# Optimization experiments

Hardware: AMD Instinct MI355X
Metric: run time of the kernel (lower is better)

Reference implementation:

```python
import jax, jax.numpy as jnp
import numpy as np

MAX_DIST = 20
N_HEADS = 8
LN_EPS = 1e-5


def _layer_norm(x, g, b):
    mu = jnp.mean(x, axis=-1, keepdims=True)
    var = jnp.var(x, axis=-1, keepdims=True)
    return (x - mu) / jnp.sqrt(var + LN_EPS) * g + b


def setup_inputs() -> dict:
    key = jax.random.key(0)
    ks = jax.random.split(key, 12)
    B, N, D, H, F = 8, 1024, 768, N_HEADS, 1024
    w = lambda k, *sh: (jax.random.normal(k, sh, jnp.float32) * 0.02)
    return {
        "x": jax.random.normal(ks[0], (B, N, D), jnp.float32),
        "node_mask": jnp.ones((B, N), jnp.int32),
        "centers": jnp.arange(B * N, dtype=jnp.float32).reshape(B, N),
        "types": jax.random.randint(ks[1], (B, N), 0, 2, jnp.int32),
        # params (torch Linear weights stored transposed as [in, out])
        "qkv_w": w(ks[2], D, 3 * D), "qkv_b": jnp.zeros((3 * D,), jnp.float32),
        "out_w": w(ks[3], D, D), "out_b": jnp.zeros((D,), jnp.float32),
        "ff1_w": w(ks[4], D, F), "ff1_b": jnp.zeros((F,), jnp.float32),
        "ff2_w": w(ks[5], F, D), "ff2_b": jnp.zeros((D,), jnp.float32),
        "ln1_g": jnp.ones((D,), jnp.float32), "ln1_b": jnp.zeros((D,), jnp.float32),
        "ln2_g": jnp.ones((D,), jnp.float32), "ln2_b": jnp.zeros((D,), jnp.float32),
        "rel_emb": w(ks[6], 2 * MAX_DIST + 1, H),  # relative-distance bias table
        "tt": w(ks[7], H, 2, 2),                   # type-pair bias table
    }


def reference(x, node_mask, centers, types,
              qkv_w, qkv_b, out_w, out_b,
              ff1_w, ff1_b, ff2_w, ff2_b,
              ln1_g, ln1_b, ln2_g, ln2_b,
              rel_emb, tt):
    B, N, D = x.shape
    H = rel_emb.shape[1]
    Dh = D // H

    qkv = x @ qkv_w + qkv_b                       # [B,N,3D]
    q, k, v = jnp.split(qkv, 3, axis=-1)
    split = lambda t: t.reshape(B, N, H, Dh).transpose(0, 2, 1, 3)  # [B,H,N,Dh]
    q, k, v = split(q), split(k), split(v)

    scores = jnp.einsum("bhid,bhjd->bhij", q, k) / np.sqrt(Dh).astype(np.float32)

    # relative-position bias: bucket clamped distance into [0, 2*max_dist]
    dist = centers[:, :, None] - centers[:, None, :]              # [B,N,N]
    idx = jnp.round(jnp.clip(dist, -MAX_DIST, MAX_DIST) + MAX_DIST).astype(jnp.int32)
    rb = rel_emb[idx].transpose(0, 3, 1, 2)                       # [B,H,N,N]

    # type-pair bias
    ti = jnp.broadcast_to(types[:, :, None], (B, N, N))
    tj = jnp.broadcast_to(types[:, None, :], (B, N, N))
    tb = tt[:, ti, tj].transpose(1, 0, 2, 3)                      # [B,H,N,N]

    scores = scores + rb + tb
    mask = node_mask[:, None, None, :]                            # [B,1,1,N]
    scores = jnp.where(mask == 0, -jnp.inf, scores)
    att = jax.nn.softmax(scores, axis=-1)
    att = jnp.nan_to_num(att, nan=0.0)

    y = jnp.einsum("bhij,bhjd->bhid", att, v)
    y = y.transpose(0, 2, 1, 3).reshape(B, N, D)
    y = y @ out_w + out_b

    x = _layer_norm(x + y, ln1_g, ln1_b)
    ff = jax.nn.gelu(x @ ff1_w + ff1_b, approximate=False) @ ff2_w + ff2_b
    x = _layer_norm(x + ff, ln2_g, ln2_b)
    return x
```

## Files before the change

### kernel.cpp

```cpp
#include <hip/hip_runtime.h>

typedef short short8 __attribute__((ext_vector_type(8)));
typedef unsigned short ushort8v __attribute__((ext_vector_type(8)));
typedef float f32x4 __attribute__((ext_vector_type(4)));

static __device__ __forceinline__ unsigned short f2b(float f) {
    unsigned int u = __builtin_bit_cast(unsigned int, f);
    unsigned int r = (u + 0x7fffu + ((u >> 16) & 1u)) >> 16;
    return (unsigned short)r;
}
static __device__ __forceinline__ unsigned short f2b_trunc(float f) {
    return (unsigned short)(__builtin_bit_cast(unsigned int, f) >> 16);
}
static __device__ __forceinline__ float b2f(unsigned short u) {
    return __builtin_bit_cast(float, (unsigned int)u << 16);
}
static __device__ __forceinline__ float exp2v(float x) {
    float r;
    asm("v_exp_f32 %0, %1" : "=v"(r) : "v"(x));
    return r;
}

__device__ __forceinline__ void gload16(void* lds, const void* g) {
    __builtin_amdgcn_global_load_lds(
        (const __attribute__((address_space(1))) void*)g,
        (__attribute__((address_space(3))) void*)lds, 16, 0, 0);
}

#define L2E 1.4426950408889634f

__global__ __launch_bounds__(256) void cvt_x_kernel(const float* __restrict__ x,
                                                    unsigned short* __restrict__ o, int n4) {
    int i = blockIdx.x * 256 + threadIdx.x;
    float4 f = ((const float4*)x)[i];
    ushort4 u;
    u.x = f2b(f.x); u.y = f2b(f.y); u.z = f2b(f.z); u.w = f2b(f.w);
    ((ushort4*)o)[i] = u;
}

__global__ __launch_bounds__(256) void transpose_w(const float* __restrict__ W,
                                                   unsigned short* __restrict__ Wt,
                                                   int K, int N) {
    __shared__ float t[32][33];
    int kb = blockIdx.y << 5, nb = blockIdx.x << 5;
    int tx = threadIdx.x & 31, ty = threadIdx.x >> 5;
#pragma unroll
    for (int i = 0; i < 32; i += 8)
        t[ty + i][tx] = W[(size_t)(kb + ty + i) * N + nb + tx];
    __syncthreads();
#pragma unroll
    for (int i = 0; i < 32; i += 8)
        Wt[(size_t)(nb + ty + i) * K + kb + tx] = f2b(t[tx][ty + i]);
}

__global__ __launch_bounds__(256) void aug_qk(const int* __restrict__ types,
                                              const int* __restrict__ nmask,
                                              const float* __restrict__ tt,
                                              unsigned short* __restrict__ Qb,
                                              unsigned short* __restrict__ Kb) {
    int t = blockIdx.x * 256 + threadIdx.x;
    int bh = t >> 10, n = t & 1023;
    int b = bh >> 3, h = bh & 7;
    int tj = types[b * 1024 + n];
    int mk = nmask[b * 1024 + n];
    float t00 = tt[h * 4], t01 = tt[h * 4 + 1], t10 = tt[h * 4 + 2], t11 = tt[h * 4 + 3];
    float bA = L2E * (t00 + (t01 - t00) * tj) + (mk ? 0.f : -1e30f);
    float bB = L2E * ((t10 - t00) + (t11 - t01 - t10 + t00) * tj);
    size_t off = ((size_t)bh * 1024 + n) * 128 + 96;
    ushort8v z = {0, 0, 0, 0, 0, 0, 0, 0};
    ushort8v qv = z, kv = z;
    qv[0] = 0x3F80u;
    qv[1] = tj ? 0x3F80u : 0u;
    kv[0] = f2b(bA);
    kv[1] = f2b(bB);
    *(ushort8v*)&Qb[off] = qv;
    *(ushort8v*)&Qb[off + 8] = z;
    *(ushort8v*)&Qb[off + 16] = z;
    *(ushort8v*)&Qb[off + 24] = z;
    *(ushort8v*)&Kb[off] = kv;
    *(ushort8v*)&Kb[off + 8] = z;
    *(ushort8v*)&Kb[off + 16] = z;
    *(ushort8v*)&Kb[off + 24] = z;
}

template <int EPI>
__global__ __launch_bounds__(512, 4) void gemm2p(
    const unsigned short* __restrict__ A, const unsigned short* __restrict__ Bt,
    const float* __restrict__ bias, float* __restrict__ outf,
    unsigned short* __restrict__ outb, unsigned short* __restrict__ q_o,
    unsigned short* __restrict__ k_o, unsigned short* __restrict__ v_o,
    int N, int K, int ntn, int NT) {
    __shared__ unsigned short a_lds[2][8192];
    __shared__ unsigned short b_lds[2][8192];
    const int tid = threadIdx.x;
    const int wave = tid >> 6, lane = tid & 63;
    const int lr = lane & 15, lg = lane >> 4;
    const int wm = wave >> 2, wn = wave & 3;
    const int nwg = gridDim.x;
    const int orig = blockIdx.x;
    const int swz = (orig & 7) * (nwg >> 3) + (orig >> 3);
    const int tm = swz / ntn, tn = swz % ntn;

    const unsigned short* srcA[2];
    const unsigned short* srcB[2];
#pragma unroll
    for (int i = 0; i < 2; ++i) {
        int g = i * 512 + tid;
        int row = g >> 3, sl = g & 7;
        int colg = sl ^ (row & 7);
        srcA[i] = A + (size_t)(tm * 128 + row) * K + colg * 8;
        srcB[i] = Bt + (size_t)(tn * 128 + row) * K + colg * 8;
    }
    auto stage = [&](int buf, int k0) {
#pragma unroll
        for (int i = 0; i < 2; ++i) {
            gload16(&a_lds[buf][i * 4096 + wave * 512], srcA[i] + k0);
            gload16(&b_lds[buf][i * 4096 + wave * 512], srcB[i] + k0);
        }
    };

    f32x4 acc[4][2] = {};

    stage(0, 0);
    asm volatile("s_waitcnt vmcnt(0)" ::: "memory");
    __builtin_amdgcn_s_barrier();

    for (int t = 0; t < NT; ++t) {
        const int buf = t & 1;
        if (t + 1 < NT) stage(buf ^ 1, (t + 1) * 64);
#pragma unroll
        for (int ks = 0; ks < 2; ++ks) {
            short8 af[4], bfr[2];
#pragma unroll
            for (int mf = 0; mf < 4; ++mf) {
                int row = wm * 64 + mf * 16 + lr;
                int slot = (ks * 4 + lg) ^ (row & 7);
                af[mf] = *(const short8*)&a_lds[buf][row * 64 + slot * 8];
            }
#pragma unroll
            for (int nf = 0; nf < 2; ++nf) {
                int row = wn * 32 + nf * 16 + lr;
                int slot = (ks * 4 + lg) ^ (row & 7);
                bfr[nf] = *(const short8*)&b_lds[buf][row * 64 + slot * 8];
            }
#pragma unroll
            for (int mf = 0; mf < 4; ++mf)
#pragma unroll
                for (int nf = 0; nf < 2; ++nf)
                    acc[mf][nf] = __builtin_amdgcn_mfma_f32_16x16x32_bf16(af[mf], bfr[nf], acc[mf][nf], 0, 0, 0);
        }
        asm volatile("s_waitcnt vmcnt(0)" ::: "memory");
        __builtin_amdgcn_s_barrier();
    }

#pragma unroll
    for (int nf = 0; nf < 2; ++nf) {
        int gc = tn * 128 + wn * 32 + nf * 16 + lr;
        float bv = bias[gc];
        int part = 0, h = 0, dh = 0;
        if constexpr (EPI == 3) {
            part = gc / 768;
            int cc = gc - part * 768;
            h = cc / 96;
            dh = cc - h * 96;
        }
#pragma unroll
        for (int mf = 0; mf < 4; ++mf) {
            int grb = tm * 128 + wm * 64 + mf * 16 + lg * 4;
            if constexpr (EPI == 3) {
                int b = grb >> 10, n2 = grb & 1023;
                size_t bh = (size_t)(b * 8 + h);
                if (part == 2) {
                    ushort4 wv;
                    wv.x = f2b(acc[mf][nf][0] + bv);
                    wv.y = f2b(acc[mf][nf][1] + bv);
                    wv.z = f2b(acc[mf][nf][2] + bv);
                    wv.w = f2b(acc[mf][nf][3] + bv);
                    *(ushort4*)&v_o[(bh * 96 + dh) * 1024 + n2] = wv;
                } else {
                    unsigned short* dst = (part == 0) ? q_o : k_o;
                    float sc = (part == 0) ? 0.14724445f : 1.f;
#pragma unroll
                    for (int r = 0; r < 4; ++r)
                        dst[(bh * 1024 + n2 + r) * 128 + dh] = f2b((acc[mf][nf][r] + bv) * sc);
                }
            } else {
#pragma unroll
                for (int r = 0; r < 4; ++r) {
                    int gr = grb + r;
                    float v = acc[mf][nf][r] + bv;
                    if constexpr (EPI == 0) {
                        outf[(size_t)gr * N + gc] = v;
                    } else if constexpr (EPI == 1) {
                        outb[(size_t)gr * N + gc] = f2b(v);
                    } else {
                        float gl = 0.5f * v * (1.f + erff(v * 0.70710678f));
                        outb[(size_t)gr * N + gc] = f2b(gl);
                    }
                }
            }
        }
    }
}

__global__ __launch_bounds__(512, 4) void attn_kernel(
    const unsigned short* __restrict__ Qb, const unsigned short* __restrict__ Kb,
    const unsigned short* __restrict__ Vt, const float* __restrict__ centers,
    const float* __restrict__ rel_emb, unsigned short* __restrict__ Y) {
    __shared__ unsigned short kv_lds[2 * 14336];
    __shared__ unsigned short p_lds[8 * 1024];
    __shared__ float c_lds[1024];
    __shared__ float rel_lds[41];

    const int tid = threadIdx.x;
    const int wave = tid >> 6, lane = tid & 63;
    const int lr = lane & 15, lg = lane >> 4;
    const int bh = blockIdx.x, qb = blockIdx.y;
    const int b = bh >> 3, h = bh & 7;
    const int q0 = qb * 128 + wave * 16;
    const size_t kvbase = (size_t)bh * 1024 * 128;

    c_lds[tid] = centers[b * 1024 + tid];
    c_lds[tid + 512] = centers[b * 1024 + 512 + tid];
    if (tid < 41) rel_lds[tid] = rel_emb[tid * 8 + h] * L2E;

    const unsigned short* sbase[4];
    int sstep[4];
#pragma unroll
    for (int it = 0; it < 4; ++it) {
        int g = (it < 3) ? it * 512 + tid : 1536 + wave * 64 + lane;
        if (g < 1024) {
            int ks = g >> 8, rem = g & 255, pr = rem >> 3, sl = rem & 7;
            int so = sl ^ (pr & 7);
            int r = ((so >> 2) << 5) + pr, oct = so & 3;
            sbase[it] = Kb + kvbase + (size_t)r * 128 + ks * 32 + oct * 8;
            sstep[it] = 64 * 128;
        } else {
            int v = g - 1024, pr = v >> 3, sl = v & 7;
            int so = sl ^ (pr & 7);
            sbase[it] = Vt + (size_t)(bh * 96 + (pr < 96 ? pr : 95)) * 1024 + so * 8;
            sstep[it] = 64;
        }
    }
    auto stage = [&](int bufb, int kt) {
        unsigned short* dst = kv_lds + bufb * 14336;
#pragma unroll
        for (int it = 0; it < 3; ++it)
            gload16(dst + it * 4096 + wave * 512, sbase[it] + (size_t)kt * sstep[it]);
        if (tid < 256)
            gload16(dst + 3 * 4096 + wave * 512, sbase[3] + (size_t)kt * sstep[3]);
    };

    short8 qa[4];
#pragma unroll
    for (int ks = 0; ks < 4; ++ks)
        qa[ks] = *(const short8*)&Qb[kvbase + (size_t)(q0 + lr) * 128 + ks * 32 + lg * 8];
    float ci20[4];
#pragma unroll
    for (int r = 0; r < 4; ++r) ci20[r] = centers[b * 1024 + q0 + lg * 4 + r] + 20.f;

    short8 vone = {};
    if (lr == 0) {
#pragma unroll
        for (int e = 0; e < 8; ++e) vone[e] = (short)0x3F80;
    }

    float m_r[4] = {-3e30f, -3e30f, -3e30f, -3e30f};
    f32x4 oacc[7] = {};

    stage(0, 0);
    asm volatile("s_waitcnt lgkmcnt(0)" ::: "memory");

    for (int kt = 0; kt < 16; ++kt) {
        const int buf = kt & 1;
        if (kt < 15) {
            stage(buf ^ 1, kt + 1);
            asm volatile("s_waitcnt vmcnt(3)" ::: "memory");
        } else {
            asm volatile("s_waitcnt vmcnt(0)" ::: "memory");
        }
        __builtin_amdgcn_s_barrier();
        const unsigned short* kv = kv_lds + buf * 14336;

        f32x4 s[4] = {};
#pragma unroll
        for (int jf = 0; jf < 4; ++jf) {
            int pr = ((jf & 1) << 4) + lr;
            int slp = (((jf >> 1) << 2) + lg) ^ (lr & 7);
#pragma unroll
            for (int ks = 0; ks < 4; ++ks) {
                short8 kf = *(const short8*)&kv[ks * 2048 + pr * 64 + slp * 8];
                s[jf] = __builtin_amdgcn_mfma_f32_16x16x32_bf16(qa[ks], kf, s[jf], 0, 0, 0);
            }
        }

#pragma unroll
        for (int jf = 0; jf < 4; ++jf) {
            float cj = c_lds[kt * 64 + jf * 16 + lr];
#pragma unroll
            for (int r = 0; r < 4; ++r) {
                float idxf = __builtin_amdgcn_fmed3f(ci20[r] - cj, 0.f, 40.f);
                s[jf][r] += rel_lds[(int)rintf(idxf)];
            }
        }

#pragma unroll
        for (int r = 0; r < 4; ++r) {
            float mx = fmaxf(fmaxf(s[0][r], s[1][r]), fmaxf(s[2][r], s[3][r]));
#pragma unroll
            for (int off = 1; off < 16; off <<= 1) mx = fmaxf(mx, __shfl_xor(mx, off));
            if (!__all(mx <= m_r[r] + 8.f)) {
                float mn = fmaxf(m_r[r], mx);
                float al = exp2v(m_r[r] - mn);
                m_r[r] = mn;
#pragma unroll
                for (int nf = 0; nf < 7; ++nf) oacc[nf][r] *= al;
            }
#pragma unroll
            for (int jf = 0; jf < 4; ++jf) s[jf][r] = exp2v(s[jf][r] - m_r[r]);
        }

#pragma unroll
        for (int jf = 0; jf < 4; ++jf)
#pragma unroll
            for (int r = 0; r < 4; ++r) {
                int row = lg * 4 + r, col = jf * 16 + lr;
                int gp = (col >> 3) ^ (row & 7);
                p_lds[wave * 1024 + row * 64 + gp * 8 + (col & 7)] = f2b_trunc(s[jf][r]);
            }
        asm volatile("s_waitcnt lgkmcnt(0)" ::: "memory");
        short8 pa[2];
#pragma unroll
        for (int js = 0; js < 2; ++js) {
            int slp = ((js << 2) + lg) ^ (lr & 7);
            pa[js] = *(const short8*)&p_lds[wave * 1024 + lr * 64 + slp * 8];
        }

#pragma unroll
        for (int nf = 0; nf < 6; ++nf) {
            int vrow = nf * 16 + lr;
#pragma unroll
            for (int js = 0; js < 2; ++js) {
                int slp = ((js << 2) + lg) ^ (lr & 7);
                short8 vf = *(const short8*)&kv[8192 + vrow * 64 + slp * 8];
                oacc[nf] = __builtin_amdgcn_mfma_f32_16x16x32_bf16(pa[js], vf, oacc[nf], 0, 0, 0);
            }
        }
#pragma unroll
        for (int js = 0; js < 2; ++js)
            oacc[6] = __builtin_amdgcn_mfma_f32_16x16x32_bf16(pa[js], vone, oacc[6], 0, 0, 0);
        __builtin_amdgcn_s_barrier();
    }

#pragma unroll
    for (int r = 0; r < 4; ++r) {
        float l = __shfl(oacc[6][r], lane & 48);
        float inv = (l > 0.f) ? 1.f / l : 0.f;
        int qi = q0 + lg * 4 + r;
#pragma unroll
        for (int nf = 0; nf < 6; ++nf)
            Y[((size_t)b * 1024 + qi) * 768 + h * 96 + nf * 16 + lr] = f2b(oacc[nf][r] * inv);
    }
}

template <bool IN1BF, bool IN2BF>
__global__ __launch_bounds__(384) void ln_kernel(const void* __restrict__ in1,
                                                 const void* __restrict__ in2,
                                                 const float* __restrict__ g,
                                                 const float* __restrict__ be,
                                                 float* __restrict__ of,
                                                 unsigned short* __restrict__ ob) {
    const int tid = threadIdx.x;
    const int half = tid / 192;
    const int t = tid - half * 192;
    const int row = blockIdx.x * 2 + half;
    const size_t base = (size_t)row * 768 + t * 4;
    float a[4], bb[4];
    if (IN1BF) {
        ushort4 u = *(const ushort4*)((const unsigned short*)in1 + base);
        a[0] = b2f(u.x); a[1] = b2f(u.y); a[2] = b2f(u.z); a[3] = b2f(u.w);
    } else {
        float4 u = *(const float4*)((const float*)in1 + base);
        a[0] = u.x; a[1] = u.y; a[2] = u.z; a[3] = u.w;
    }
    if (IN2BF) {
        ushort4 u = *(const ushort4*)((const unsigned short*)in2 + base);
        bb[0] = b2f(u.x); bb[1] = b2f(u.y); bb[2] = b2f(u.z); bb[3] = b2f(u.w);
    } else {
        float4 u = *(const float4*)((const float*)in2 + base);
        bb[0] = u.x; bb[1] = u.y; bb[2] = u.z; bb[3] = u.w;
    }
    float v[4];
#pragma unroll
    for (int i = 0; i < 4; ++i) v[i] = a[i] + bb[i];
    float s1 = v[0] + v[1] + v[2] + v[3];
    float s2 = v[0] * v[0] + v[1] * v[1] + v[2] * v[2] + v[3] * v[3];
#pragma unroll
    for (int off = 32; off > 0; off >>= 1) {
        s1 += __shfl_xor(s1, off);
        s2 += __shfl_xor(s2, off);
    }
    __shared__ float red[12];
    const int wv = tid >> 6;
    if ((tid & 63) == 0) { red[wv] = s1; red[6 + wv] = s2; }
    __syncthreads();
    const int w0 = half * 3;
    s1 = red[w0] + red[w0 + 1] + red[w0 + 2];
    s2 = red[6 + w0] + red[6 + w0 + 1] + red[6 + w0 + 2];
    float mu = s1 * (1.f / 768.f);
    float var = s2 * (1.f / 768.f) - mu * mu;
    float inv = rsqrtf(var + 1e-5f);
    float o[4];
#pragma unroll
    for (int i = 0; i < 4; ++i)
        o[i] = (v[i] - mu) * inv * g[t * 4 + i] + be[t * 4 + i];
    if (of) {
        float4 w = {o[0], o[1], o[2], o[3]};
        *(float4*)(of + base) = w;
    }
    if (ob) {
        ushort4 w = {f2b(o[0]), f2b(o[1]), f2b(o[2]), f2b(o[3])};
        *(ushort4*)(ob + base) = w;
    }
}

extern "C" void kernel_launch(void* const* d_in, const int* in_sizes, int n_in,
                              void* d_out, int out_size, void* d_ws, size_t ws_size,
                              hipStream_t stream) {
    const float* x     = (const float*)d_in[0];
    const int*   nmask = (const int*)d_in[1];
    const float* cent  = (const float*)d_in[2];
    const int*   types = (const int*)d_in[3];
    const float* qkv_w = (const float*)d_in[4];
    const float* qkv_b = (const float*)d_in[5];
    const float* out_w = (const float*)d_in[6];
    const float* out_b = (const float*)d_in[7];
    const float* ff1_w = (const float*)d_in[8];
    const float* ff1_b = (const float*)d_in[9];
    const float* ff2_w = (const float*)d_in[10];
    const float* ff2_b = (const float*)d_in[11];
    const float* ln1_g = (const float*)d_in[12];
    const float* ln1_b = (const float*)d_in[13];
    const float* ln2_g = (const float*)d_in[14];
    const float* ln2_b = (const float*)d_in[15];
    const float* rel   = (const float*)d_in[16];
    const float* ttp   = (const float*)d_in[17];

    char* w = (char*)d_ws;
    auto alloc = [&](size_t bytes) {
        char* p = w;
        w += (bytes + 255) & ~(size_t)255;
        return p;
    };
    unsigned short* xb  = (unsigned short*)alloc(8192ull * 768 * 2);
    unsigned short* qwT = (unsigned short*)alloc(2304ull * 768 * 2);
    unsigned short* owT = (unsigned short*)alloc(768ull * 768 * 2);
    unsigned short* f1T = (unsigned short*)alloc(1024ull * 768 * 2);
    unsigned short* f2T = (unsigned short*)alloc(768ull * 1024 * 2);
    unsigned short* Qb  = (unsigned short*)alloc(64ull * 1024 * 128 * 2);
    unsigned short* Kb  = (unsigned short*)alloc(64ull * 1024 * 128 * 2);
    unsigned short* Vt  = (unsigned short*)alloc(64ull * 96 * 1024 * 2);
    unsigned short* aob = (unsigned short*)alloc(8192ull * 768 * 2);
    unsigned short* h1b = (unsigned short*)alloc(8192ull * 768 * 2);
    unsigned short* ffa = Qb;

    cvt_x_kernel<<<6144, 256, 0, stream>>>(x, xb, 8192 * 768 / 4);
    transpose_w<<<dim3(2304 / 32, 768 / 32), 256, 0, stream>>>(qkv_w, qwT, 768, 2304);
    transpose_w<<<dim3(768 / 32, 768 / 32), 256, 0, stream>>>(out_w, owT, 768, 768);
    transpose_w<<<dim3(1024 / 32, 768 / 32), 256, 0, stream>>>(ff1_w, f1T, 768, 1024);
    transpose_w<<<dim3(768 / 32, 1024 / 32), 256, 0, stream>>>(ff2_w, f2T, 1024, 768);

    gemm2p<3><<<1152, 512, 0, stream>>>(xb, qwT, qkv_b, nullptr, nullptr,
                                        Qb, Kb, Vt, 2304, 768, 18, 12);
    aug_qk<<<256, 256, 0, stream>>>(types, nmask, ttp, Qb, Kb);
    attn_kernel<<<dim3(64, 8), 512, 0, stream>>>(Qb, Kb, Vt, cent, rel, xb);
    gemm2p<1><<<384, 512, 0, stream>>>(xb, owT, out_b, nullptr, aob,
                                       nullptr, nullptr, nullptr, 768, 768, 6, 12);
    ln_kernel<false, true><<<4096, 384, 0, stream>>>(x, aob, ln1_g, ln1_b, nullptr, h1b);
    gemm2p<2><<<512, 512, 0, stream>>>(h1b, f1T, ff1_b, nullptr, ffa,
                                       nullptr, nullptr, nullptr, 1024, 768, 8, 12);
    gemm2p<1><<<384, 512, 0, stream>>>(ffa, f2T, ff2_b, nullptr, aob,
                                       nullptr, nullptr, nullptr, 768, 1024, 6, 16);
    ln_kernel<true, true><<<4096, 384, 0, stream>>>(h1b, aob, ln2_g, ln2_b, (float*)d_out, nullptr);
}
```

Measured before the change: 214.1 us.

## Process two query tiles per attention wave and merge prep kernels

The attention kernel now runs 4 waves of 256 threads, each handling 32 query rows (two 16-row MFMA tiles), so every K and V fragment read from LDS feeds two MFMAs. This halves K/V LDS reads per unit of compute, at the cost of higher register use per wave and fewer waves to hide latency. Staging is redistributed across 7 loads per thread, with the V row clamp removed. Separately, the x conversion and the four weight transposes are merged into a single launch to cut launch overhead.

```diff
diff --git a/kernel.cpp b/kernel.cpp
--- a/kernel.cpp
+++ b/kernel.cpp
@@ -29,21 +29,32 @@
 
 #define L2E 1.4426950408889634f
 
-__global__ __launch_bounds__(256) void cvt_x_kernel(const float* __restrict__ x,
-                                                    unsigned short* __restrict__ o, int n4) {
-    int i = blockIdx.x * 256 + threadIdx.x;
-    float4 f = ((const float4*)x)[i];
-    ushort4 u;
-    u.x = f2b(f.x); u.y = f2b(f.y); u.z = f2b(f.z); u.w = f2b(f.w);
-    ((ushort4*)o)[i] = u;
-}
-
-__global__ __launch_bounds__(256) void transpose_w(const float* __restrict__ W,
-                                                   unsigned short* __restrict__ Wt,
-                                                   int K, int N) {
+__global__ __launch_bounds__(256) void prep_kernel(
+    const float* __restrict__ x, unsigned short* __restrict__ xb,
+    const float* __restrict__ qkv_w, unsigned short* __restrict__ qwT,
+    const float* __restrict__ out_w, unsigned short* __restrict__ owT,
+    const float* __restrict__ ff1_w, unsigned short* __restrict__ f1T,
+    const float* __restrict__ ff2_w, unsigned short* __restrict__ f2T) {
+    const int bx = blockIdx.x;
+    const int tid = threadIdx.x;
+    if (bx < 6144) {
+        int i = bx * 256 + tid;
+        float4 f = ((const float4*)x)[i];
+        ushort4 u;
+        u.x = f2b(f.x); u.y = f2b(f.y); u.z = f2b(f.z); u.w = f2b(f.w);
+        ((ushort4*)xb)[i] = u;
+        return;
+    }
     __shared__ float t[32][33];
-    int kb = blockIdx.y << 5, nb = blockIdx.x << 5;
-    int tx = threadIdx.x & 31, ty = threadIdx.x >> 5;
+    int rb = bx - 6144;
+    const float* W; unsigned short* Wt; int K, N;
+    if (rb < 1728)      { W = qkv_w; Wt = qwT; K = 768;  N = 2304; }
+    else if (rb < 2304) { rb -= 1728; W = out_w; Wt = owT; K = 768;  N = 768; }
+    else if (rb < 3072) { rb -= 2304; W = ff1_w; Wt = f1T; K = 768;  N = 1024; }
+    else                { rb -= 3072; W = ff2_w; Wt = f2T; K = 1024; N = 768; }
+    const int nbl = N / 32;
+    const int nb = (rb % nbl) * 32, kb = (rb / nbl) * 32;
+    const int tx = tid & 31, ty = tid >> 5;
 #pragma unroll
     for (int i = 0; i < 32; i += 8)
         t[ty + i][tx] = W[(size_t)(kb + ty + i) * N + nb + tx];
@@ -203,12 +214,12 @@
     }
 }
 
-__global__ __launch_bounds__(512, 4) void attn_kernel(
+__global__ __launch_bounds__(256, 2) void attn_kernel(
     const unsigned short* __restrict__ Qb, const unsigned short* __restrict__ Kb,
     const unsigned short* __restrict__ Vt, const float* __restrict__ centers,
     const float* __restrict__ rel_emb, unsigned short* __restrict__ Y) {
     __shared__ unsigned short kv_lds[2 * 14336];
-    __shared__ unsigned short p_lds[8 * 1024];
+    __shared__ unsigned short p_lds[4 * 2048];
     __shared__ float c_lds[1024];
     __shared__ float rel_lds[41];
 
@@ -217,18 +228,19 @@
     const int lr = lane & 15, lg = lane >> 4;
     const int bh = blockIdx.x, qb = blockIdx.y;
     const int b = bh >> 3, h = bh & 7;
-    const int q0 = qb * 128 + wave * 16;
+    const int q0 = qb * 128 + wave * 32;
     const size_t kvbase = (size_t)bh * 1024 * 128;
 
-    c_lds[tid] = centers[b * 1024 + tid];
-    c_lds[tid + 512] = centers[b * 1024 + 512 + tid];
+#pragma unroll
+    for (int i = 0; i < 4; ++i)
+        c_lds[tid + i * 256] = centers[b * 1024 + tid + i * 256];
     if (tid < 41) rel_lds[tid] = rel_emb[tid * 8 + h] * L2E;
 
-    const unsigned short* sbase[4];
-    int sstep[4];
-#pragma unroll
-    for (int it = 0; it < 4; ++it) {
-        int g = (it < 3) ? it * 512 + tid : 1536 + wave * 64 + lane;
+    const unsigned short* sbase[7];
+    int sstep[7];
+#pragma unroll
+    for (int it = 0; it < 7; ++it) {
+        int g = it * 256 + tid;
         if (g < 1024) {
             int ks = g >> 8, rem = g & 255, pr = rem >> 3, sl = rem & 7;
             int so = sl ^ (pr & 7);
@@ -238,26 +250,29 @@
         } else {
             int v = g - 1024, pr = v >> 3, sl = v & 7;
             int so = sl ^ (pr & 7);
-            sbase[it] = Vt + (size_t)(bh * 96 + (pr < 96 ? pr : 95)) * 1024 + so * 8;
+            sbase[it] = Vt + (size_t)(bh * 96 + pr) * 1024 + so * 8;
             sstep[it] = 64;
         }
     }
     auto stage = [&](int bufb, int kt) {
         unsigned short* dst = kv_lds + bufb * 14336;
 #pragma unroll
-        for (int it = 0; it < 3; ++it)
-            gload16(dst + it * 4096 + wave * 512, sbase[it] + (size_t)kt * sstep[it]);
-        if (tid < 256)
-            gload16(dst + 3 * 4096 + wave * 512, sbase[3] + (size_t)kt * sstep[3]);
+        for (int it = 0; it < 7; ++it)
+            gload16(dst + it * 2048 + wave * 512, sbase[it] + (size_t)kt * sstep[it]);
     };
 
-    short8 qa[4];
-#pragma unroll
-    for (int ks = 0; ks < 4; ++ks)
-        qa[ks] = *(const short8*)&Qb[kvbase + (size_t)(q0 + lr) * 128 + ks * 32 + lg * 8];
-    float ci20[4];
-#pragma unroll
-    for (int r = 0; r < 4; ++r) ci20[r] = centers[b * 1024 + q0 + lg * 4 + r] + 20.f;
+    short8 qa[2][4];
+#pragma unroll
+    for (int h2 = 0; h2 < 2; ++h2)
+#pragma unroll
+        for (int ks = 0; ks < 4; ++ks)
+            qa[h2][ks] = *(const short8*)&Qb[kvbase + (size_t)(q0 + h2 * 16 + lr) * 128 + ks * 32 + lg * 8];
+    float ci20[2][4];
+#pragma unroll
+    for (int h2 = 0; h2 < 2; ++h2)
+#pragma unroll
+        for (int r = 0; r < 4; ++r)
+            ci20[h2][r] = centers[b * 1024 + q0 + h2 * 16 + lg * 4 + r] + 20.f;
 
     short8 vone = {};
     if (lr == 0) {
@@ -265,8 +280,8 @@
         for (int e = 0; e < 8; ++e) vone[e] = (short)0x3F80;
     }
 
-    float m_r[4] = {-3e30f, -3e30f, -3e30f, -3e30f};
-    f32x4 oacc[7] = {};
+    float m_r[2][4] = {{-3e30f, -3e30f, -3e30f, -3e30f}, {-3e30f, -3e30f, -3e30f, -3e30f}};
+    f32x4 oacc[2][7] = {};
 
     stage(0, 0);
     asm volatile("s_waitcnt lgkmcnt(0)" ::: "memory");
@@ -275,14 +290,14 @@
         const int buf = kt & 1;
         if (kt < 15) {
             stage(buf ^ 1, kt + 1);
-            asm volatile("s_waitcnt vmcnt(3)" ::: "memory");
+            asm volatile("s_waitcnt vmcnt(7)" ::: "memory");
         } else {
             asm volatile("s_waitcnt vmcnt(0)" ::: "memory");
         }
         __builtin_amdgcn_s_barrier();
         const unsigned short* kv = kv_lds + buf * 14336;
 
-        f32x4 s[4] = {};
+        f32x4 s[2][4] = {};
 #pragma unroll
         for (int jf = 0; jf < 4; ++jf) {
             int pr = ((jf & 1) << 4) + lr;
@@ -290,7 +305,8 @@
 #pragma unroll
             for (int ks = 0; ks < 4; ++ks) {
                 short8 kf = *(const short8*)&kv[ks * 2048 + pr * 64 + slp * 8];
-                s[jf] = __builtin_amdgcn_mfma_f32_16x16x32_bf16(qa[ks], kf, s[jf], 0, 0, 0);
+                s[0][jf] = __builtin_amdgcn_mfma_f32_16x16x32_bf16(qa[0][ks], kf, s[0][jf], 0, 0, 0);
+                s[1][jf] = __builtin_amdgcn_mfma_f32_16x16x32_bf16(qa[1][ks], kf, s[1][jf], 0, 0, 0);
             }
         }
 
@@ -298,43 +314,51 @@
         for (int jf = 0; jf < 4; ++jf) {
             float cj = c_lds[kt * 64 + jf * 16 + lr];
 #pragma unroll
+            for (int h2 = 0; h2 < 2; ++h2)
+#pragma unroll
+                for (int r = 0; r < 4; ++r) {
+                    float idxf = __builtin_amdgcn_fmed3f(ci20[h2][r] - cj, 0.f, 40.f);
+                    s[h2][jf][r] += rel_lds[(int)rintf(idxf)];
+                }
+        }
+
+#pragma unroll
+        for (int h2 = 0; h2 < 2; ++h2)
+#pragma unroll
             for (int r = 0; r < 4; ++r) {
-                float idxf = __builtin_amdgcn_fmed3f(ci20[r] - cj, 0.f, 40.f);
-                s[jf][r] += rel_lds[(int)rintf(idxf)];
-            }
-        }
-
-#pragma unroll
-        for (int r = 0; r < 4; ++r) {
-            float mx = fmaxf(fmaxf(s[0][r], s[1][r]), fmaxf(s[2][r], s[3][r]));
-#pragma unroll
-            for (int off = 1; off < 16; off <<= 1) mx = fmaxf(mx, __shfl_xor(mx, off));
-            if (!__all(mx <= m_r[r] + 8.f)) {
-                float mn = fmaxf(m_r[r], mx);
-                float al = exp2v(m_r[r] - mn);
-                m_r[r] = mn;
-#pragma unroll
-                for (int nf = 0; nf < 7; ++nf) oacc[nf][r] *= al;
-            }
-#pragma unroll
-            for (int jf = 0; jf < 4; ++jf) s[jf][r] = exp2v(s[jf][r] - m_r[r]);
-        }
-
-#pragma unroll
-        for (int jf = 0; jf < 4; ++jf)
-#pragma unroll
-            for (int r = 0; r < 4; ++r) {
-                int row = lg * 4 + r, col = jf * 16 + lr;
-                int gp = (col >> 3) ^ (row & 7);
-                p_lds[wave * 1024 + row * 64 + gp * 8 + (col & 7)] = f2b_trunc(s[jf][r]);
-            }
+                float mx = fmaxf(fmaxf(s[h2][0][r], s[h2][1][r]), fmaxf(s[h2][2][r], s[h2][3][r]));
+#pragma unroll
+                for (int off = 1; off < 16; off <<= 1) mx = fmaxf(mx, __shfl_xor(mx, off));
+                if (!__all(mx <= m_r[h2][r] + 8.f)) {
+                    float mn = fmaxf(m_r[h2][r], mx);
+                    float al = exp2v(m_r[h2][r] - mn);
+                    m_r[h2][r] = mn;
+#pragma unroll
+                    for (int nf = 0; nf < 7; ++nf) oacc[h2][nf][r] *= al;
+                }
+#pragma unroll
+                for (int jf = 0; jf < 4; ++jf) s[h2][jf][r] = exp2v(s[h2][jf][r] - m_r[h2][r]);
+            }
+
+#pragma unroll
+        for (int h2 = 0; h2 < 2; ++h2)
+#pragma unroll
+            for (int jf = 0; jf < 4; ++jf)
+#pragma unroll
+                for (int r = 0; r < 4; ++r) {
+                    int row = lg * 4 + r, col = jf * 16 + lr;
+                    int gp = (col >> 3) ^ (row & 7);
+                    p_lds[wave * 2048 + h2 * 1024 + row * 64 + gp * 8 + (col & 7)] = f2b_trunc(s[h2][jf][r]);
+                }
         asm volatile("s_waitcnt lgkmcnt(0)" ::: "memory");
-        short8 pa[2];
-#pragma unroll
-        for (int js = 0; js < 2; ++js) {
-            int slp = ((js << 2) + lg) ^ (lr & 7);
-            pa[js] = *(const short8*)&p_lds[wave * 1024 + lr * 64 + slp * 8];
-        }
+        short8 pa[2][2];
+#pragma unroll
+        for (int h2 = 0; h2 < 2; ++h2)
+#pragma unroll
+            for (int js = 0; js < 2; ++js) {
+                int slp = ((js << 2) + lg) ^ (lr & 7);
+                pa[h2][js] = *(const short8*)&p_lds[wave * 2048 + h2 * 1024 + lr * 64 + slp * 8];
+            }
 
 #pragma unroll
         for (int nf = 0; nf < 6; ++nf) {
@@ -343,24 +367,29 @@
             for (int js = 0; js < 2; ++js) {
                 int slp = ((js << 2) + lg) ^ (lr & 7);
                 short8 vf = *(const short8*)&kv[8192 + vrow * 64 + slp * 8];
-                oacc[nf] = __builtin_amdgcn_mfma_f32_16x16x32_bf16(pa[js], vf, oacc[nf], 0, 0, 0);
-            }
-        }
-#pragma unroll
-        for (int js = 0; js < 2; ++js)
-            oacc[6] = __builtin_amdgcn_mfma_f32_16x16x32_bf16(pa[js], vone, oacc[6], 0, 0, 0);
+                oacc[0][nf] = __builtin_amdgcn_mfma_f32_16x16x32_bf16(pa[0][js], vf, oacc[0][nf], 0, 0, 0);
+                oacc[1][nf] = __builtin_amdgcn_mfma_f32_16x16x32_bf16(pa[1][js], vf, oacc[1][nf], 0, 0, 0);
+            }
+        }
+#pragma unroll
+        for (int h2 = 0; h2 < 2; ++h2)
+#pragma unroll
+            for (int js = 0; js < 2; ++js)
+                oacc[h2][6] = __builtin_amdgcn_mfma_f32_16x16x32_bf16(pa[h2][js], vone, oacc[h2][6], 0, 0, 0);
         __builtin_amdgcn_s_barrier();
     }
 
 #pragma unroll
-    for (int r = 0; r < 4; ++r) {
-        float l = __shfl(oacc[6][r], lane & 48);
-        float inv = (l > 0.f) ? 1.f / l : 0.f;
-        int qi = q0 + lg * 4 + r;
-#pragma unroll
-        for (int nf = 0; nf < 6; ++nf)
-            Y[((size_t)b * 1024 + qi) * 768 + h * 96 + nf * 16 + lr] = f2b(oacc[nf][r] * inv);
-    }
+    for (int h2 = 0; h2 < 2; ++h2)
+#pragma unroll
+        for (int r = 0; r < 4; ++r) {
+            float l = __shfl(oacc[h2][6][r], lane & 48);
+            float inv = (l > 0.f) ? 1.f / l : 0.f;
+            int qi = q0 + h2 * 16 + lg * 4 + r;
+#pragma unroll
+            for (int nf = 0; nf < 6; ++nf)
+                Y[((size_t)b * 1024 + qi) * 768 + h * 96 + nf * 16 + lr] = f2b(oacc[h2][nf][r] * inv);
+        }
 }
 
 template <bool IN1BF, bool IN2BF>
@@ -464,16 +493,13 @@
     unsigned short* h1b = (unsigned short*)alloc(8192ull * 768 * 2);
     unsigned short* ffa = Qb;
 
-    cvt_x_kernel<<<6144, 256, 0, stream>>>(x, xb, 8192 * 768 / 4);
-    transpose_w<<<dim3(2304 / 32, 768 / 32), 256, 0, stream>>>(qkv_w, qwT, 768, 2304);
-    transpose_w<<<dim3(768 / 32, 768 / 32), 256, 0, stream>>>(out_w, owT, 768, 768);
-    transpose_w<<<dim3(1024 / 32, 768 / 32), 256, 0, stream>>>(ff1_w, f1T, 768, 1024);
-    transpose_w<<<dim3(768 / 32, 1024 / 32), 256, 0, stream>>>(ff2_w, f2T, 1024, 768);
+    prep_kernel<<<9984, 256, 0, stream>>>(x, xb, qkv_w, qwT, out_w, owT,
+                                          ff1_w, f1T, ff2_w, f2T);
 
     gemm2p<3><<<1152, 512, 0, stream>>>(xb, qwT, qkv_b, nullptr, nullptr,
                                         Qb, Kb, Vt, 2304, 768, 18, 12);
     aug_qk<<<256, 256, 0, stream>>>(types, nmask, ttp, Qb, Kb);
-    attn_kernel<<<dim3(64, 8), 512, 0, stream>>>(Qb, Kb, Vt, cent, rel, xb);
+    attn_kernel<<<dim3(64, 8), 256, 0, stream>>>(Qb, Kb, Vt, cent, rel, xb);
     gemm2p<1><<<384, 512, 0, stream>>>(xb, owT, out_b, nullptr, aob,
                                        nullptr, nullptr, nullptr, 768, 768, 6, 12);
     ln_kernel<false, true><<<4096, 384, 0, stream>>>(x, aob, ln1_g, ln1_b, nullptr, h1b);
```

After: 211.0 us. Within noise of the previous version (-1.4%).

## Drop padded QK bias columns, compute type/mask bias in attention, merge prep kernels

Applied to the files above, without the earlier changes.

Q and K are now stored with a head dimension of 96 instead of 128. The type-pair and mask bias is no longer written into padding columns by a separate aug_qk kernel. Instead, attention builds packed bias pairs in LDS and applies them through one extra small MFMA per key fragment, which cuts Q/K memory traffic and LDS staging, lowers LDS footprint, and removes a launch. The x conversion and the four weight transposes are merged into one prep kernel to save launch overhead. In exchange, attention does extra LDS reads and per-block bias setup, and the prep kernel has divergent block roles.

```diff
diff --git a/kernel.cpp b/kernel.cpp
--- a/kernel.cpp
+++ b/kernel.cpp
@@ -29,21 +29,32 @@
 
 #define L2E 1.4426950408889634f
 
-__global__ __launch_bounds__(256) void cvt_x_kernel(const float* __restrict__ x,
-                                                    unsigned short* __restrict__ o, int n4) {
-    int i = blockIdx.x * 256 + threadIdx.x;
-    float4 f = ((const float4*)x)[i];
-    ushort4 u;
-    u.x = f2b(f.x); u.y = f2b(f.y); u.z = f2b(f.z); u.w = f2b(f.w);
-    ((ushort4*)o)[i] = u;
-}
-
-__global__ __launch_bounds__(256) void transpose_w(const float* __restrict__ W,
-                                                   unsigned short* __restrict__ Wt,
-                                                   int K, int N) {
+__global__ __launch_bounds__(256) void prep_kernel(
+    const float* __restrict__ x, unsigned short* __restrict__ xb,
+    const float* __restrict__ qkv_w, unsigned short* __restrict__ qwT,
+    const float* __restrict__ out_w, unsigned short* __restrict__ owT,
+    const float* __restrict__ ff1_w, unsigned short* __restrict__ f1T,
+    const float* __restrict__ ff2_w, unsigned short* __restrict__ f2T) {
+    const int bx = blockIdx.x;
+    const int tid = threadIdx.x;
+    if (bx < 6144) {
+        int i = bx * 256 + tid;
+        float4 f = ((const float4*)x)[i];
+        ushort4 u;
+        u.x = f2b(f.x); u.y = f2b(f.y); u.z = f2b(f.z); u.w = f2b(f.w);
+        ((ushort4*)xb)[i] = u;
+        return;
+    }
     __shared__ float t[32][33];
-    int kb = blockIdx.y << 5, nb = blockIdx.x << 5;
-    int tx = threadIdx.x & 31, ty = threadIdx.x >> 5;
+    int rb = bx - 6144;
+    const float* W; unsigned short* Wt; int K, N;
+    if (rb < 1728)      { W = qkv_w; Wt = qwT; K = 768;  N = 2304; }
+    else if (rb < 2304) { rb -= 1728; W = out_w; Wt = owT; K = 768;  N = 768; }
+    else if (rb < 3072) { rb -= 2304; W = ff1_w; Wt = f1T; K = 768;  N = 1024; }
+    else                { rb -= 3072; W = ff2_w; Wt = f2T; K = 1024; N = 768; }
+    const int nbl = N / 32;
+    const int nb = (rb % nbl) * 32, kb = (rb / nbl) * 32;
+    const int tx = tid & 31, ty = tid >> 5;
 #pragma unroll
     for (int i = 0; i < 32; i += 8)
         t[ty + i][tx] = W[(size_t)(kb + ty + i) * N + nb + tx];
@@ -51,36 +62,6 @@
 #pragma unroll
     for (int i = 0; i < 32; i += 8)
         Wt[(size_t)(nb + ty + i) * K + kb + tx] = f2b(t[tx][ty + i]);
-}
-
-__global__ __launch_bounds__(256) void aug_qk(const int* __restrict__ types,
-                                              const int* __restrict__ nmask,
-                                              const float* __restrict__ tt,
-                                              unsigned short* __restrict__ Qb,
-                                              unsigned short* __restrict__ Kb) {
-    int t = blockIdx.x * 256 + threadIdx.x;
-    int bh = t >> 10, n = t & 1023;
-    int b = bh >> 3, h = bh & 7;
-    int tj = types[b * 1024 + n];
-    int mk = nmask[b * 1024 + n];
-    float t00 = tt[h * 4], t01 = tt[h * 4 + 1], t10 = tt[h * 4 + 2], t11 = tt[h * 4 + 3];
-    float bA = L2E * (t00 + (t01 - t00) * tj) + (mk ? 0.f : -1e30f);
-    float bB = L2E * ((t10 - t00) + (t11 - t01 - t10 + t00) * tj);
-    size_t off = ((size_t)bh * 1024 + n) * 128 + 96;
-    ushort8v z = {0, 0, 0, 0, 0, 0, 0, 0};
-    ushort8v qv = z, kv = z;
-    qv[0] = 0x3F80u;
-    qv[1] = tj ? 0x3F80u : 0u;
-    kv[0] = f2b(bA);
-    kv[1] = f2b(bB);
-    *(ushort8v*)&Qb[off] = qv;
-    *(ushort8v*)&Qb[off + 8] = z;
-    *(ushort8v*)&Qb[off + 16] = z;
-    *(ushort8v*)&Qb[off + 24] = z;
-    *(ushort8v*)&Kb[off] = kv;
-    *(ushort8v*)&Kb[off + 8] = z;
-    *(ushort8v*)&Kb[off + 16] = z;
-    *(ushort8v*)&Kb[off + 24] = z;
 }
 
 template <int EPI>
@@ -182,7 +163,7 @@
                     float sc = (part == 0) ? 0.14724445f : 1.f;
 #pragma unroll
                     for (int r = 0; r < 4; ++r)
-                        dst[(bh * 1024 + n2 + r) * 128 + dh] = f2b((acc[mf][nf][r] + bv) * sc);
+                        dst[(bh * 1024 + n2 + r) * 96 + dh] = f2b((acc[mf][nf][r] + bv) * sc);
                 }
             } else {
 #pragma unroll
@@ -206,10 +187,13 @@
 __global__ __launch_bounds__(512, 4) void attn_kernel(
     const unsigned short* __restrict__ Qb, const unsigned short* __restrict__ Kb,
     const unsigned short* __restrict__ Vt, const float* __restrict__ centers,
-    const float* __restrict__ rel_emb, unsigned short* __restrict__ Y) {
-    __shared__ unsigned short kv_lds[2 * 14336];
+    const int* __restrict__ types, const int* __restrict__ nmask,
+    const float* __restrict__ tt, const float* __restrict__ rel_emb,
+    unsigned short* __restrict__ Y) {
+    __shared__ unsigned short kv_lds[2 * 12288];
     __shared__ unsigned short p_lds[8 * 1024];
     __shared__ float c_lds[1024];
+    __shared__ unsigned int bab_lds[1024];
     __shared__ float rel_lds[41];
 
     const int tid = threadIdx.x;
@@ -218,43 +202,62 @@
     const int bh = blockIdx.x, qb = blockIdx.y;
     const int b = bh >> 3, h = bh & 7;
     const int q0 = qb * 128 + wave * 16;
-    const size_t kvbase = (size_t)bh * 1024 * 128;
+    const size_t kvbase = (size_t)bh * 1024 * 96;
 
     c_lds[tid] = centers[b * 1024 + tid];
     c_lds[tid + 512] = centers[b * 1024 + 512 + tid];
     if (tid < 41) rel_lds[tid] = rel_emb[tid * 8 + h] * L2E;
-
-    const unsigned short* sbase[4];
-    int sstep[4];
-#pragma unroll
-    for (int it = 0; it < 4; ++it) {
-        int g = (it < 3) ? it * 512 + tid : 1536 + wave * 64 + lane;
-        if (g < 1024) {
+    {
+        const float t00 = tt[h * 4], t01 = tt[h * 4 + 1];
+        const float t10 = tt[h * 4 + 2], t11 = tt[h * 4 + 3];
+#pragma unroll
+        for (int i = 0; i < 2; ++i) {
+            int j = tid + i * 512;
+            int tj = types[b * 1024 + j];
+            int mk = nmask[b * 1024 + j];
+            float bA = L2E * (t00 + (t01 - t00) * tj) + (mk ? 0.f : -1e30f);
+            float bB = L2E * ((t10 - t00) + (t11 - t01 - t10 + t00) * tj);
+            bab_lds[j] = (unsigned)f2b(bA) | ((unsigned)f2b(bB) << 16);
+        }
+    }
+
+    const unsigned short* sbase[3];
+    int sstep[3];
+#pragma unroll
+    for (int it = 0; it < 3; ++it) {
+        int g = it * 512 + tid;
+        if (g < 768) {
             int ks = g >> 8, rem = g & 255, pr = rem >> 3, sl = rem & 7;
             int so = sl ^ (pr & 7);
             int r = ((so >> 2) << 5) + pr, oct = so & 3;
-            sbase[it] = Kb + kvbase + (size_t)r * 128 + ks * 32 + oct * 8;
-            sstep[it] = 64 * 128;
+            sbase[it] = Kb + kvbase + (size_t)r * 96 + ks * 32 + oct * 8;
+            sstep[it] = 64 * 96;
         } else {
-            int v = g - 1024, pr = v >> 3, sl = v & 7;
+            int gv = g - 768, pr = gv >> 3, sl = gv & 7;
             int so = sl ^ (pr & 7);
-            sbase[it] = Vt + (size_t)(bh * 96 + (pr < 96 ? pr : 95)) * 1024 + so * 8;
+            sbase[it] = Vt + (size_t)(bh * 96 + pr) * 1024 + so * 8;
             sstep[it] = 64;
         }
     }
     auto stage = [&](int bufb, int kt) {
-        unsigned short* dst = kv_lds + bufb * 14336;
+        unsigned short* dst = kv_lds + bufb * 12288;
 #pragma unroll
         for (int it = 0; it < 3; ++it)
             gload16(dst + it * 4096 + wave * 512, sbase[it] + (size_t)kt * sstep[it]);
-        if (tid < 256)
-            gload16(dst + 3 * 4096 + wave * 512, sbase[3] + (size_t)kt * sstep[3]);
     };
 
-    short8 qa[4];
-#pragma unroll
-    for (int ks = 0; ks < 4; ++ks)
-        qa[ks] = *(const short8*)&Qb[kvbase + (size_t)(q0 + lr) * 128 + ks * 32 + lg * 8];
+    short8 qa[3];
+#pragma unroll
+    for (int ks = 0; ks < 3; ++ks)
+        qa[ks] = *(const short8*)&Qb[kvbase + (size_t)(q0 + lr) * 96 + ks * 32 + lg * 8];
+    short8 qa3 = {};
+    {
+        int ti0 = types[b * 1024 + q0 + lr];
+        if (lg == 0) {
+            qa3[0] = (short)0x3F80;
+            qa3[1] = ti0 ? (short)0x3F80 : (short)0;
+        }
+    }
     float ci20[4];
 #pragma unroll
     for (int r = 0; r < 4; ++r) ci20[r] = centers[b * 1024 + q0 + lg * 4 + r] + 20.f;
@@ -280,7 +283,7 @@
             asm volatile("s_waitcnt vmcnt(0)" ::: "memory");
         }
         __builtin_amdgcn_s_barrier();
-        const unsigned short* kv = kv_lds + buf * 14336;
+        const unsigned short* kv = kv_lds + buf * 12288;
 
         f32x4 s[4] = {};
 #pragma unroll
@@ -288,10 +291,17 @@
             int pr = ((jf & 1) << 4) + lr;
             int slp = (((jf >> 1) << 2) + lg) ^ (lr & 7);
 #pragma unroll
-            for (int ks = 0; ks < 4; ++ks) {
+            for (int ks = 0; ks < 3; ++ks) {
                 short8 kf = *(const short8*)&kv[ks * 2048 + pr * 64 + slp * 8];
                 s[jf] = __builtin_amdgcn_mfma_f32_16x16x32_bf16(qa[ks], kf, s[jf], 0, 0, 0);
             }
+            unsigned vb = bab_lds[kt * 64 + jf * 16 + lr];
+            short8 kf3 = {};
+            if (lg == 0) {
+                kf3[0] = (short)(vb & 0xffffu);
+                kf3[1] = (short)(vb >> 16);
+            }
+            s[jf] = __builtin_amdgcn_mfma_f32_16x16x32_bf16(qa3, kf3, s[jf], 0, 0, 0);
         }
 
 #pragma unroll
@@ -342,7 +352,7 @@
 #pragma unroll
             for (int js = 0; js < 2; ++js) {
                 int slp = ((js << 2) + lg) ^ (lr & 7);
-                short8 vf = *(const short8*)&kv[8192 + vrow * 64 + slp * 8];
+                short8 vf = *(const short8*)&kv[6144 + vrow * 64 + slp * 8];
                 oacc[nf] = __builtin_amdgcn_mfma_f32_16x16x32_bf16(pa[js], vf, oacc[nf], 0, 0, 0);
             }
         }
@@ -457,23 +467,19 @@
     unsigned short* owT = (unsigned short*)alloc(768ull * 768 * 2);
     unsigned short* f1T = (unsigned short*)alloc(1024ull * 768 * 2);
     unsigned short* f2T = (unsigned short*)alloc(768ull * 1024 * 2);
-    unsigned short* Qb  = (unsigned short*)alloc(64ull * 1024 * 128 * 2);
-    unsigned short* Kb  = (unsigned short*)alloc(64ull * 1024 * 128 * 2);
+    unsigned short* Qb  = (unsigned short*)alloc(64ull * 1024 * 96 * 2);
+    unsigned short* Kb  = (unsigned short*)alloc(64ull * 1024 * 96 * 2);
     unsigned short* Vt  = (unsigned short*)alloc(64ull * 96 * 1024 * 2);
     unsigned short* aob = (unsigned short*)alloc(8192ull * 768 * 2);
     unsigned short* h1b = (unsigned short*)alloc(8192ull * 768 * 2);
     unsigned short* ffa = Qb;
 
-    cvt_x_kernel<<<6144, 256, 0, stream>>>(x, xb, 8192 * 768 / 4);
-    transpose_w<<<dim3(2304 / 32, 768 / 32), 256, 0, stream>>>(qkv_w, qwT, 768, 2304);
-    transpose_w<<<dim3(768 / 32, 768 / 32), 256, 0, stream>>>(out_w, owT, 768, 768);
-    transpose_w<<<dim3(1024 / 32, 768 / 32), 256, 0, stream>>>(ff1_w, f1T, 768, 1024);
-    transpose_w<<<dim3(768 / 32, 1024 / 32), 256, 0, stream>>>(ff2_w, f2T, 1024, 768);
+    prep_kernel<<<9984, 256, 0, stream>>>(x, xb, qkv_w, qwT, out_w, owT,
+                                          ff1_w, f1T, ff2_w, f2T);
 
     gemm2p<3><<<1152, 512, 0, stream>>>(xb, qwT, qkv_b, nullptr, nullptr,
                                         Qb, Kb, Vt, 2304, 768, 18, 12);
-    aug_qk<<<256, 256, 0, stream>>>(types, nmask, ttp, Qb, Kb);
-    attn_kernel<<<dim3(64, 8), 512, 0, stream>>>(Qb, Kb, Vt, cent, rel, xb);
+    attn_kernel<<<dim3(64, 8), 512, 0, stream>>>(Qb, Kb, Vt, cent, types, nmask, ttp, rel, xb);
     gemm2p<1><<<384, 512, 0, stream>>>(xb, owT, out_b, nullptr, aob,
                                        nullptr, nullptr, nullptr, 768, 768, 6, 12);
     ln_kernel<false, true><<<4096, 384, 0, stream>>>(x, aob, ln1_g, ln1_b, nullptr, h1b);
```

Measured after the change: 202.8 us. 5.3% less time.
